# Kernel optimization log

Hardware: AMD Instinct MI355X
Metric: run time of the kernel (lower is better)

Reference implementation:

```python
import jax, jax.numpy as jnp
import numpy as np

N_NODES = 100000
N_EDGES = 1600000
DIM = 128


def setup_inputs() -> dict:
    key = jax.random.key(0)
    k1, k2, k3, k4 = jax.random.split(key, 4)
    x = jax.random.normal(k1, (N_NODES, DIM), dtype=jnp.float32)
    edge_index = jax.random.randint(k2, (2, N_EDGES), 0, N_NODES, dtype=jnp.int64)
    # PyG GCNConv params: Linear weight [out, in] (glorot) and bias [out] (zeros -> use small randn for a non-trivial grad path)
    W = jax.random.normal(k3, (DIM, DIM), dtype=jnp.float32) * (1.0 / np.sqrt(DIM))
    b = jax.random.normal(k4, (DIM,), dtype=jnp.float32) * 0.01
    return {"x": x, "edge_index": edge_index, "W": W, "b": b}


def reference(x, edge_index, W, b):
    # Faithful GCNConv: add self-loops, symmetric deg^-1/2 normalization,
    # linear transform, scatter-add aggregation, bias.
    N = x.shape[0]
    loop = jnp.arange(N, dtype=edge_index.dtype)
    src = jnp.concatenate([edge_index[0], loop])  # [E+N]
    dst = jnp.concatenate([edge_index[1], loop])  # [E+N]

    # degree (with self-loops) on destination nodes
    deg = jax.ops.segment_sum(jnp.ones_like(dst, dtype=x.dtype), dst, num_segments=N)
    dinv = jnp.where(deg > 0, jax.lax.rsqrt(deg), 0.0)
    norm = dinv[src] * dinv[dst]  # [E+N]

    x_lin = x @ W.T  # [N, dim] — PyG applies linear before propagate
    msg = x_lin[src] * norm[:, None]  # [E+N, dim] gather + scale
    out = jax.ops.segment_sum(msg, dst, num_segments=N)  # scatter-add aggregate
    return out + b
```

## Files before the change

kernel.cpp:

```cpp
#include <hip/hip_runtime.h>
#include <hip/hip_bf16.h>


#define DIM 128
#define BINSHIFT 9
#define BINSZ 512
#define NB 196
#define MAXNB 256
#define CAPB 16384
#define WSTRIDE 136
#define SCAT_BLOCKS 256

typedef __attribute__((ext_vector_type(8))) short short8;
typedef __attribute__((ext_vector_type(4))) float f32x4;
typedef __attribute__((ext_vector_type(4))) unsigned short ushort4v;

__device__ inline unsigned short f2bf(float f) {
    unsigned u = __builtin_bit_cast(unsigned, f);
    return (unsigned short)((u + 0x7FFFu + ((u >> 16) & 1u)) >> 16);
}

__device__ inline void bf8_axpy(uint4 v, float s, float* acc) {
    acc[0] = fmaf(s, __builtin_bit_cast(float, v.x << 16), acc[0]);
    acc[1] = fmaf(s, __builtin_bit_cast(float, v.x & 0xFFFF0000u), acc[1]);
    acc[2] = fmaf(s, __builtin_bit_cast(float, v.y << 16), acc[2]);
    acc[3] = fmaf(s, __builtin_bit_cast(float, v.y & 0xFFFF0000u), acc[3]);
    acc[4] = fmaf(s, __builtin_bit_cast(float, v.z << 16), acc[4]);
    acc[5] = fmaf(s, __builtin_bit_cast(float, v.z & 0xFFFF0000u), acc[5]);
    acc[6] = fmaf(s, __builtin_bit_cast(float, v.w << 16), acc[6]);
    acc[7] = fmaf(s, __builtin_bit_cast(float, v.w & 0xFFFF0000u), acc[7]);
}

__global__ __launch_bounds__(256) void scatter_wconv(const int* __restrict__ ei, int E,
                                                     int* __restrict__ binCursor,
                                                     int2* __restrict__ binned,
                                                     const float* __restrict__ W,
                                                     unsigned short* __restrict__ wbf) {
    int t = threadIdx.x;
    if (blockIdx.x >= SCAT_BLOCKS) {
        int base = (blockIdx.x - SCAT_BLOCKS) * 1024 + t * 4;
#pragma unroll
        for (int i = 0; i < 4; ++i) {
            float4 w4 = ((const float4*)W)[base + i];
            ushort4v o; o.x = f2bf(w4.x); o.y = f2bf(w4.y); o.z = f2bf(w4.z); o.w = f2bf(w4.w);
            ((ushort4v*)wbf)[base + i] = o;
        }
        return;
    }
    __shared__ int lh[MAXNB];
    __shared__ int lbase[MAXNB];
    lh[t] = 0;
    __syncthreads();
    int chunk = (E + SCAT_BLOCKS - 1) / SCAT_BLOCKS;
    int base = blockIdx.x * chunk, end = min(E, base + chunk);
    for (int i = base + t; i < end; i += 256)
        atomicAdd(&lh[ei[E + i] >> BINSHIFT], 1);
    __syncthreads();
    if (t < NB) {
        int c = lh[t];
        lbase[t] = c ? atomicAdd(&binCursor[t], c) : 0;
        lh[t] = 0;
    }
    __syncthreads();
    for (int i = base + t; i < end; i += 256) {
        int s = ei[i], d = ei[E + i];
        int b = d >> BINSHIFT;
        int pos = b * CAPB + lbase[b] + atomicAdd(&lh[b], 1);
        binned[pos] = make_int2(s, d);
    }
}


__global__ __launch_bounds__(256) void csr_gemm(const int2* __restrict__ binned,
                                                const int* __restrict__ binCursor,
                                                int* __restrict__ col,
                                                int2* __restrict__ rowinfo,
                                                float* __restrict__ dinv,
                                                const float* __restrict__ x,
                                                const unsigned short* __restrict__ wbf,
                                                unsigned short* __restrict__ xlin, int N) {
    __shared__ unsigned short obuf[4 * 16 * WSTRIDE];
    __shared__ int ldeg[BINSZ], sa[BINSZ], sb[BINSZ], lcur[BINSZ];
    int t = threadIdx.x;

    if (blockIdx.x < NB) {
        int b = blockIdx.x;
        int s0 = b * CAPB;
        int s1 = s0 + binCursor[b];
        for (int i = t; i < BINSZ; i += 256) { ldeg[i] = 0; lcur[i] = 0; }
        __syncthreads();
        for (int i = s0 + t; i < s1; i += 256)
            atomicAdd(&ldeg[binned[i].y & (BINSZ - 1)], 1);
        __syncthreads();
        for (int i = t; i < BINSZ; i += 256) sa[i] = ldeg[i];
        __syncthreads();
        int* src = sa; int* dstp = sb;
        for (int step = 1; step < BINSZ; step <<= 1) {
            for (int i = t; i < BINSZ; i += 256) {
                int v = src[i];
                if (i >= step) v += src[i - step];
                dstp[i] = v;
            }
            __syncthreads();
            int* tmp = src; src = dstp; dstp = tmp;
        }
        for (int i = t; i < BINSZ; i += 256) dstp[i] = src[i] - ldeg[i];
        __syncthreads();
        for (int i = t; i < BINSZ; i += 256) {
            int n = (b << BINSHIFT) + i;
            if (n < N) {
                rowinfo[n] = make_int2(s0 + dstp[i], ldeg[i]);
                dinv[n] = rsqrtf((float)(ldeg[i] + 1));
            }
        }
        for (int i = s0 + t; i < s1; i += 256) {
            int2 e = binned[i];
            int li = e.y & (BINSZ - 1);
            col[s0 + dstp[li] + atomicAdd(&lcur[li], 1)] = e.x;
        }
        return;
    }

    int wid = t >> 6, lane = t & 63;
    int m = lane & 15, quad = lane >> 4;
    int row_base = (blockIdx.x - NB) * 64 + wid * 16;

    f32x4 acc[8];
#pragma unroll
    for (int j = 0; j < 8; ++j) acc[j] = (f32x4){0.f, 0.f, 0.f, 0.f};

    int arow = row_base + m;
    if (arow >= N) arow = N - 1;
    const float* xr = x + (size_t)arow * DIM + quad * 8;

#pragma unroll
    for (int kc = 0; kc < 4; ++kc) {
        float4 a0 = *(const float4*)(xr + kc * 32);
        float4 a1 = *(const float4*)(xr + kc * 32 + 4);
        short8 af;
        af[0] = (short)f2bf(a0.x); af[1] = (short)f2bf(a0.y);
        af[2] = (short)f2bf(a0.z); af[3] = (short)f2bf(a0.w);
        af[4] = (short)f2bf(a1.x); af[5] = (short)f2bf(a1.y);
        af[6] = (short)f2bf(a1.z); af[7] = (short)f2bf(a1.w);
#pragma unroll
        for (int jt = 0; jt < 8; ++jt) {
            short8 bf = *(const short8*)&wbf[(jt * 16 + m) * DIM + kc * 32 + quad * 8];
            acc[jt] = __builtin_amdgcn_mfma_f32_16x16x32_bf16(af, bf, acc[jt], 0, 0, 0);
        }
    }

    unsigned short* ob = &obuf[wid * 16 * WSTRIDE];
#pragma unroll
    for (int jt = 0; jt < 8; ++jt)
#pragma unroll
        for (int r = 0; r < 4; ++r)
            ob[(quad * 4 + r) * WSTRIDE + jt * 16 + m] = f2bf(acc[jt][r]);
#pragma unroll
    for (int it = 0; it < 4; ++it) {
        int idx = it * 64 + lane;
        int r = idx >> 4;
        int cb = idx & 15;
        int grow = row_base + r;
        if (grow < N) {
            short8 v = *(const short8*)&ob[r * WSTRIDE + cb * 8];
            *(short8*)(xlin + (size_t)grow * DIM + cb * 8) = v;
        }
    }
}


__global__ __launch_bounds__(256) void aggregate(const unsigned short* __restrict__ xlin,
                                                 const int* __restrict__ col,
                                                 const int2* __restrict__ rowinfo,
                                                 const float* __restrict__ dinv,
                                                 const float* __restrict__ bias,
                                                 float* __restrict__ out, int N) {
    int node = blockIdx.x * 16 + (threadIdx.x >> 4);
    int lane = threadIdx.x & 15;
    if (node >= N) return;

    float di = dinv[node];
    int2 ri = rowinfo[node];
    int r0 = ri.x, r1 = ri.x + ri.y;

    const uint4* xl = (const uint4*)xlin;
    float acc[8] = {};
    bf8_axpy(xl[(size_t)node * 16 + lane], di, acc);

    for (int i = r0; i < r1; i += 4) {
        int rem = r1 - i;
        int s0 = col[i];
        int s1 = col[rem > 1 ? i + 1 : i];
        int s2 = col[rem > 2 ? i + 2 : i];
        int s3 = col[rem > 3 ? i + 3 : i];
        float d0 = dinv[s0];
        float d1 = rem > 1 ? dinv[s1] : 0.f;
        float d2 = rem > 2 ? dinv[s2] : 0.f;
        float d3 = rem > 3 ? dinv[s3] : 0.f;
        uint4 v0 = xl[(size_t)s0 * 16 + lane];
        uint4 v1 = xl[(size_t)s1 * 16 + lane];
        uint4 v2 = xl[(size_t)s2 * 16 + lane];
        uint4 v3 = xl[(size_t)s3 * 16 + lane];
        bf8_axpy(v0, d0, acc);
        bf8_axpy(v1, d1, acc);
        bf8_axpy(v2, d2, acc);
        bf8_axpy(v3, d3, acc);
    }

    const float4* b4 = (const float4*)(bias + lane * 8);
    float4 bl = b4[0], bh = b4[1];
    float4 olo = make_float4(di * acc[0] + bl.x, di * acc[1] + bl.y,
                             di * acc[2] + bl.z, di * acc[3] + bl.w);
    float4 ohi = make_float4(di * acc[4] + bh.x, di * acc[5] + bh.y,
                             di * acc[6] + bh.z, di * acc[7] + bh.w);
    float4* op = (float4*)(out + (size_t)node * DIM + lane * 8);
    op[0] = olo;
    op[1] = ohi;
}


extern "C" void kernel_launch(void* const* d_in, const int* in_sizes, int n_in,
                              void* d_out, int out_size, void* d_ws, size_t ws_size,
                              hipStream_t stream) {
    const float* x    = (const float*)d_in[0];
    const int*   ei   = (const int*)d_in[1];
    const float* W    = (const float*)d_in[2];
    const float* bias = (const float*)d_in[3];
    float* out = (float*)d_out;

    const int N = in_sizes[0] / DIM;
    const int E = in_sizes[1] / 2;

    char* ws = (char*)d_ws;
    size_t off = 0;
    auto alloc = [&](size_t bytes) { size_t o = off; off = (off + bytes + 255) & ~(size_t)255; return o; };
    unsigned short* xlin = (unsigned short*)(ws + alloc((size_t)N * DIM * 2));
    int2* binned   = (int2*) (ws + alloc((size_t)NB * CAPB * 8));
    int*  col      = (int*)  (ws + alloc((size_t)NB * CAPB * 4));
    int2* rowinfo  = (int2*) (ws + alloc((size_t)N * 8));
    float* dinv    = (float*)(ws + alloc((size_t)N * 4));
    int*  binCursor= (int*)  (ws + alloc(MAXNB * 4));
    unsigned short* wbf = (unsigned short*)(ws + alloc((size_t)DIM * DIM * 2));

    hipMemsetAsync(binCursor, 0, MAXNB * 4, stream);
    scatter_wconv<<<SCAT_BLOCKS + 4, 256, 0, stream>>>(ei, E, binCursor, binned, W, wbf);
    csr_gemm<<<NB + (N + 63) / 64, 256, 0, stream>>>(
        binned, binCursor, col, rowinfo, dinv, x, wbf, xlin, N);
    aggregate<<<(N + 15) / 16, 256, 0, stream>>>(xlin, col, rowinfo, dinv, bias, out, N);
}
```

Baseline: 227.6 us.

## Build CSR via global degree histogram and atomic cursor placement instead of binning

Replaces the two-pass bin-then-sort CSR construction with a global per-node degree histogram (global atomics), a per-bin scan kernel that writes row starts and dinv, and an atomic-cursor placement of source indices fused into the GEMM launch. This drops the intermediate binned edge array and its extra read/write pass. In exchange it relies on heavily contended global atomics over 1.6M edges, adds a kernel launch and an N-sized memset, and makes the order of neighbours within each row nondeterministic.

Result: slower. 334.6 us (+47.0%).

```diff
diff --git a/kernel.cpp b/kernel.cpp
--- a/kernel.cpp
+++ b/kernel.cpp
@@ -6,10 +6,8 @@
 #define BINSHIFT 9
 #define BINSZ 512
 #define NB 196
-#define MAXNB 256
 #define CAPB 16384
 #define WSTRIDE 136
-#define SCAT_BLOCKS 256
 
 typedef __attribute__((ext_vector_type(8))) short short8;
 typedef __attribute__((ext_vector_type(4))) float f32x4;
@@ -31,14 +29,15 @@
     acc[7] = fmaf(s, __builtin_bit_cast(float, v.w & 0xFFFF0000u), acc[7]);
 }
 
-__global__ __launch_bounds__(256) void scatter_wconv(const int* __restrict__ ei, int E,
-                                                     int* __restrict__ binCursor,
-                                                     int2* __restrict__ binned,
-                                                     const float* __restrict__ W,
-                                                     unsigned short* __restrict__ wbf) {
+__global__ __launch_bounds__(256) void hist_wconv(const int* __restrict__ ei, int E,
+                                                  int* __restrict__ deg,
+                                                  const float* __restrict__ W,
+                                                  unsigned short* __restrict__ wbf) {
     int t = threadIdx.x;
-    if (blockIdx.x >= SCAT_BLOCKS) {
-        int base = (blockIdx.x - SCAT_BLOCKS) * 1024 + t * 4;
+    int E4 = E >> 2;
+    int nh = (E4 + 255) >> 8;
+    if ((int)blockIdx.x >= nh) {
+        int base = ((int)blockIdx.x - nh) * 1024 + t * 4;
 #pragma unroll
         for (int i = 0; i < 4; ++i) {
             float4 w4 = ((const float4*)W)[base + i];
@@ -47,83 +46,85 @@
         }
         return;
     }
-    __shared__ int lh[MAXNB];
-    __shared__ int lbase[MAXNB];
-    lh[t] = 0;
+    int i4 = blockIdx.x * 256 + t;
+    if (i4 < E4) {
+        int4 d = ((const int4*)(ei + E))[i4];
+        atomicAdd(&deg[d.x], 1);
+        atomicAdd(&deg[d.y], 1);
+        atomicAdd(&deg[d.z], 1);
+        atomicAdd(&deg[d.w], 1);
+    }
+    if (blockIdx.x == 0 && t < (E & 3))
+        atomicAdd(&deg[ei[E + (E4 << 2) + t]], 1);
+}
+
+__global__ __launch_bounds__(256) void csrscan(int* __restrict__ degc,
+                                               int2* __restrict__ rowinfo,
+                                               float* __restrict__ dinv, int N) {
+    __shared__ int ldeg[BINSZ], sa[BINSZ], sb[BINSZ];
+    int t = threadIdx.x;
+    int b = blockIdx.x;
+    for (int i = t; i < BINSZ; i += 256) {
+        int n = (b << BINSHIFT) + i;
+        ldeg[i] = (n < N) ? degc[n] : 0;
+    }
     __syncthreads();
-    int chunk = (E + SCAT_BLOCKS - 1) / SCAT_BLOCKS;
-    int base = blockIdx.x * chunk, end = min(E, base + chunk);
-    for (int i = base + t; i < end; i += 256)
-        atomicAdd(&lh[ei[E + i] >> BINSHIFT], 1);
+    for (int i = t; i < BINSZ; i += 256) sa[i] = ldeg[i];
     __syncthreads();
-    if (t < NB) {
-        int c = lh[t];
-        lbase[t] = c ? atomicAdd(&binCursor[t], c) : 0;
-        lh[t] = 0;
-    }
-    __syncthreads();
-    for (int i = base + t; i < end; i += 256) {
-        int s = ei[i], d = ei[E + i];
-        int b = d >> BINSHIFT;
-        int pos = b * CAPB + lbase[b] + atomicAdd(&lh[b], 1);
-        binned[pos] = make_int2(s, d);
-    }
-}
-
-
-__global__ __launch_bounds__(256) void csr_gemm(const int2* __restrict__ binned,
-                                                const int* __restrict__ binCursor,
-                                                int* __restrict__ col,
-                                                int2* __restrict__ rowinfo,
-                                                float* __restrict__ dinv,
-                                                const float* __restrict__ x,
-                                                const unsigned short* __restrict__ wbf,
-                                                unsigned short* __restrict__ xlin, int N) {
+    int* src = sa; int* dstp = sb;
+    for (int step = 1; step < BINSZ; step <<= 1) {
+        for (int i = t; i < BINSZ; i += 256) {
+            int v = src[i];
+            if (i >= step) v += src[i - step];
+            dstp[i] = v;
+        }
+        __syncthreads();
+        int* tmp = src; src = dstp; dstp = tmp;
+    }
+    for (int i = t; i < BINSZ; i += 256) {
+        int n = (b << BINSHIFT) + i;
+        if (n < N) {
+            int d = ldeg[i];
+            int start = b * CAPB + src[i] - d;
+            rowinfo[n] = make_int2(start, d);
+            dinv[n] = rsqrtf((float)(d + 1));
+            degc[n] = start;
+        }
+    }
+}
+
+__global__ __launch_bounds__(256) void gemm_place(const float* __restrict__ x,
+                                                  const unsigned short* __restrict__ wbf,
+                                                  unsigned short* __restrict__ xlin,
+                                                  const int* __restrict__ ei, int E,
+                                                  int* __restrict__ cursor,
+                                                  int* __restrict__ col, int N) {
     __shared__ unsigned short obuf[4 * 16 * WSTRIDE];
-    __shared__ int ldeg[BINSZ], sa[BINSZ], sb[BINSZ], lcur[BINSZ];
     int t = threadIdx.x;
-
-    if (blockIdx.x < NB) {
-        int b = blockIdx.x;
-        int s0 = b * CAPB;
-        int s1 = s0 + binCursor[b];
-        for (int i = t; i < BINSZ; i += 256) { ldeg[i] = 0; lcur[i] = 0; }
-        __syncthreads();
-        for (int i = s0 + t; i < s1; i += 256)
-            atomicAdd(&ldeg[binned[i].y & (BINSZ - 1)], 1);
-        __syncthreads();
-        for (int i = t; i < BINSZ; i += 256) sa[i] = ldeg[i];
-        __syncthreads();
-        int* src = sa; int* dstp = sb;
-        for (int step = 1; step < BINSZ; step <<= 1) {
-            for (int i = t; i < BINSZ; i += 256) {
-                int v = src[i];
-                if (i >= step) v += src[i - step];
-                dstp[i] = v;
-            }
-            __syncthreads();
-            int* tmp = src; src = dstp; dstp = tmp;
-        }
-        for (int i = t; i < BINSZ; i += 256) dstp[i] = src[i] - ldeg[i];
-        __syncthreads();
-        for (int i = t; i < BINSZ; i += 256) {
-            int n = (b << BINSHIFT) + i;
-            if (n < N) {
-                rowinfo[n] = make_int2(s0 + dstp[i], ldeg[i]);
-                dinv[n] = rsqrtf((float)(ldeg[i] + 1));
-            }
-        }
-        for (int i = s0 + t; i < s1; i += 256) {
-            int2 e = binned[i];
-            int li = e.y & (BINSZ - 1);
-            col[s0 + dstp[li] + atomicAdd(&lcur[li], 1)] = e.x;
+    int GB = (N + 63) >> 6;
+
+    if ((int)blockIdx.x >= GB) {
+        int pb = (int)blockIdx.x - GB;
+        int E4 = E >> 2;
+        int i4 = pb * 256 + t;
+        if (i4 < E4) {
+            int4 s = ((const int4*)ei)[i4];
+            int4 d = ((const int4*)(ei + E))[i4];
+            col[atomicAdd(&cursor[d.x], 1)] = s.x;
+            col[atomicAdd(&cursor[d.y], 1)] = s.y;
+            col[atomicAdd(&cursor[d.z], 1)] = s.z;
+            col[atomicAdd(&cursor[d.w], 1)] = s.w;
+        }
+        if (pb == 0 && t < (E & 3)) {
+            int i = (E4 << 2) + t;
+            col[atomicAdd(&cursor[ei[E + i]], 1)] = ei[i];
         }
         return;
     }
 
     int wid = t >> 6, lane = t & 63;
     int m = lane & 15, quad = lane >> 4;
-    int row_base = (blockIdx.x - NB) * 64 + wid * 16;
+    int row_base = blockIdx.x * 64 + wid * 16;
 
     f32x4 acc[8];
 #pragma unroll
@@ -235,16 +236,19 @@
     size_t off = 0;
     auto alloc = [&](size_t bytes) { size_t o = off; off = (off + bytes + 255) & ~(size_t)255; return o; };
     unsigned short* xlin = (unsigned short*)(ws + alloc((size_t)N * DIM * 2));
-    int2* binned   = (int2*) (ws + alloc((size_t)NB * CAPB * 8));
     int*  col      = (int*)  (ws + alloc((size_t)NB * CAPB * 4));
     int2* rowinfo  = (int2*) (ws + alloc((size_t)N * 8));
     float* dinv    = (float*)(ws + alloc((size_t)N * 4));
-    int*  binCursor= (int*)  (ws + alloc(MAXNB * 4));
+    int*  degc     = (int*)  (ws + alloc((size_t)N * 4));
     unsigned short* wbf = (unsigned short*)(ws + alloc((size_t)DIM * DIM * 2));
 
-    hipMemsetAsync(binCursor, 0, MAXNB * 4, stream);
-    scatter_wconv<<<SCAT_BLOCKS + 4, 256, 0, stream>>>(ei, E, binCursor, binned, W, wbf);
-    csr_gemm<<<NB + (N + 63) / 64, 256, 0, stream>>>(
-        binned, binCursor, col, rowinfo, dinv, x, wbf, xlin, N);
+    int E4 = E >> 2;
+    int HB = (E4 + 255) >> 8;
+    int GB = (N + 63) >> 6;
+
+    hipMemsetAsync(degc, 0, (size_t)N * 4, stream);
+    hist_wconv<<<HB + 4, 256, 0, stream>>>(ei, E, degc, W, wbf);
+    csrscan<<<NB, 256, 0, stream>>>(degc, rowinfo, dinv, N);
+    gemm_place<<<GB + HB, 256, 0, stream>>>(x, wbf, xlin, ei, E, degc, col, N);
     aggregate<<<(N + 15) / 16, 256, 0, stream>>>(xlin, col, rowinfo, dinv, bias, out, N);
 }
```

## Regroup kernels: fuse edge scatter with GEMM, split CSR build into own kernel

Applied to the files above, without the earlier changes.

Moves the dense x·W GEMM into the same launch as the edge binning scatter, and moves the per-bin CSR construction into a separate 512-thread kernel that runs afterwards. The W bf16 conversion becomes its own tiny launch. The aim is to overlap the bandwidth-bound GEMM with the atomic-heavy scatter and to stop CSR blocks from sharing a launch with GEMM blocks. It also widens the CSR scan to one thread per node, and it adds a kernel launch plus a block barrier before the xlin store.

New measurement: 229.5 us. No clear change (+0.8%).

```diff
diff --git a/kernel.cpp b/kernel.cpp
--- a/kernel.cpp
+++ b/kernel.cpp
@@ -31,99 +31,55 @@
     acc[7] = fmaf(s, __builtin_bit_cast(float, v.w & 0xFFFF0000u), acc[7]);
 }
 
-__global__ __launch_bounds__(256) void scatter_wconv(const int* __restrict__ ei, int E,
-                                                     int* __restrict__ binCursor,
-                                                     int2* __restrict__ binned,
-                                                     const float* __restrict__ W,
-                                                     unsigned short* __restrict__ wbf) {
+__global__ __launch_bounds__(256) void wconv(const float* __restrict__ W,
+                                             unsigned short* __restrict__ wbf) {
+    int base = blockIdx.x * 1024 + threadIdx.x * 4;
+#pragma unroll
+    for (int i = 0; i < 4; ++i) {
+        float4 w4 = ((const float4*)W)[base + i];
+        ushort4v o; o.x = f2bf(w4.x); o.y = f2bf(w4.y); o.z = f2bf(w4.z); o.w = f2bf(w4.w);
+        ((ushort4v*)wbf)[base + i] = o;
+    }
+}
+
+__global__ __launch_bounds__(256) void scatter_gemm(const int* __restrict__ ei, int E,
+                                                    int* __restrict__ binCursor,
+                                                    int2* __restrict__ binned,
+                                                    const float* __restrict__ x,
+                                                    const unsigned short* __restrict__ wbf,
+                                                    unsigned short* __restrict__ xlin, int N) {
+    __shared__ __align__(16) char smem[4 * 16 * WSTRIDE * 2];
     int t = threadIdx.x;
-    if (blockIdx.x >= SCAT_BLOCKS) {
-        int base = (blockIdx.x - SCAT_BLOCKS) * 1024 + t * 4;
-#pragma unroll
-        for (int i = 0; i < 4; ++i) {
-            float4 w4 = ((const float4*)W)[base + i];
-            ushort4v o; o.x = f2bf(w4.x); o.y = f2bf(w4.y); o.z = f2bf(w4.z); o.w = f2bf(w4.w);
-            ((ushort4v*)wbf)[base + i] = o;
+
+    if (blockIdx.x < SCAT_BLOCKS) {
+        int* lh = (int*)smem;
+        int* lbase = lh + MAXNB;
+        lh[t] = 0;
+        __syncthreads();
+        int chunk = (E + SCAT_BLOCKS - 1) / SCAT_BLOCKS;
+        int base = blockIdx.x * chunk, end = min(E, base + chunk);
+        for (int i = base + t; i < end; i += 256)
+            atomicAdd(&lh[ei[E + i] >> BINSHIFT], 1);
+        __syncthreads();
+        if (t < NB) {
+            int c = lh[t];
+            lbase[t] = c ? atomicAdd(&binCursor[t], c) : 0;
+            lh[t] = 0;
+        }
+        __syncthreads();
+        for (int i = base + t; i < end; i += 256) {
+            int s = ei[i], d = ei[E + i];
+            int b = d >> BINSHIFT;
+            int pos = b * CAPB + lbase[b] + atomicAdd(&lh[b], 1);
+            binned[pos] = make_int2(s, d);
         }
         return;
     }
-    __shared__ int lh[MAXNB];
-    __shared__ int lbase[MAXNB];
-    lh[t] = 0;
-    __syncthreads();
-    int chunk = (E + SCAT_BLOCKS - 1) / SCAT_BLOCKS;
-    int base = blockIdx.x * chunk, end = min(E, base + chunk);
-    for (int i = base + t; i < end; i += 256)
-        atomicAdd(&lh[ei[E + i] >> BINSHIFT], 1);
-    __syncthreads();
-    if (t < NB) {
-        int c = lh[t];
-        lbase[t] = c ? atomicAdd(&binCursor[t], c) : 0;
-        lh[t] = 0;
-    }
-    __syncthreads();
-    for (int i = base + t; i < end; i += 256) {
-        int s = ei[i], d = ei[E + i];
-        int b = d >> BINSHIFT;
-        int pos = b * CAPB + lbase[b] + atomicAdd(&lh[b], 1);
-        binned[pos] = make_int2(s, d);
-    }
-}
-
-
-__global__ __launch_bounds__(256) void csr_gemm(const int2* __restrict__ binned,
-                                                const int* __restrict__ binCursor,
-                                                int* __restrict__ col,
-                                                int2* __restrict__ rowinfo,
-                                                float* __restrict__ dinv,
-                                                const float* __restrict__ x,
-                                                const unsigned short* __restrict__ wbf,
-                                                unsigned short* __restrict__ xlin, int N) {
-    __shared__ unsigned short obuf[4 * 16 * WSTRIDE];
-    __shared__ int ldeg[BINSZ], sa[BINSZ], sb[BINSZ], lcur[BINSZ];
-    int t = threadIdx.x;
-
-    if (blockIdx.x < NB) {
-        int b = blockIdx.x;
-        int s0 = b * CAPB;
-        int s1 = s0 + binCursor[b];
-        for (int i = t; i < BINSZ; i += 256) { ldeg[i] = 0; lcur[i] = 0; }
-        __syncthreads();
-        for (int i = s0 + t; i < s1; i += 256)
-            atomicAdd(&ldeg[binned[i].y & (BINSZ - 1)], 1);
-        __syncthreads();
-        for (int i = t; i < BINSZ; i += 256) sa[i] = ldeg[i];
-        __syncthreads();
-        int* src = sa; int* dstp = sb;
-        for (int step = 1; step < BINSZ; step <<= 1) {
-            for (int i = t; i < BINSZ; i += 256) {
-                int v = src[i];
-                if (i >= step) v += src[i - step];
-                dstp[i] = v;
-            }
-            __syncthreads();
-            int* tmp = src; src = dstp; dstp = tmp;
-        }
-        for (int i = t; i < BINSZ; i += 256) dstp[i] = src[i] - ldeg[i];
-        __syncthreads();
-        for (int i = t; i < BINSZ; i += 256) {
-            int n = (b << BINSHIFT) + i;
-            if (n < N) {
-                rowinfo[n] = make_int2(s0 + dstp[i], ldeg[i]);
-                dinv[n] = rsqrtf((float)(ldeg[i] + 1));
-            }
-        }
-        for (int i = s0 + t; i < s1; i += 256) {
-            int2 e = binned[i];
-            int li = e.y & (BINSZ - 1);
-            col[s0 + dstp[li] + atomicAdd(&lcur[li], 1)] = e.x;
-        }
-        return;
-    }
-
+
+    unsigned short* obuf = (unsigned short*)smem;
     int wid = t >> 6, lane = t & 63;
     int m = lane & 15, quad = lane >> 4;
-    int row_base = (blockIdx.x - NB) * 64 + wid * 16;
+    int row_base = (blockIdx.x - SCAT_BLOCKS) * 64 + wid * 16;
 
     f32x4 acc[8];
 #pragma unroll
@@ -155,6 +111,7 @@
 #pragma unroll
         for (int r = 0; r < 4; ++r)
             ob[(quad * 4 + r) * WSTRIDE + jt * 16 + m] = f2bf(acc[jt][r]);
+    __syncthreads();
 #pragma unroll
     for (int it = 0; it < 4; ++it) {
         int idx = it * 64 + lane;
@@ -165,6 +122,48 @@
             short8 v = *(const short8*)&ob[r * WSTRIDE + cb * 8];
             *(short8*)(xlin + (size_t)grow * DIM + cb * 8) = v;
         }
+    }
+}
+
+__global__ __launch_bounds__(512) void csr_build(const int2* __restrict__ binned,
+                                                 const int* __restrict__ binCursor,
+                                                 int* __restrict__ col,
+                                                 int2* __restrict__ rowinfo,
+                                                 float* __restrict__ dinv, int N) {
+    __shared__ int ldeg[BINSZ], sa[BINSZ], sb[BINSZ], lcur[BINSZ];
+    int t = threadIdx.x;
+    int b = blockIdx.x;
+    int s0 = b * CAPB;
+    int s1 = s0 + binCursor[b];
+
+    ldeg[t] = 0; lcur[t] = 0;
+    __syncthreads();
+    for (int i = s0 + t; i < s1; i += 512)
+        atomicAdd(&ldeg[binned[i].y & (BINSZ - 1)], 1);
+    __syncthreads();
+    sa[t] = ldeg[t];
+    __syncthreads();
+    int* src = sa; int* dstp = sb;
+    for (int step = 1; step < BINSZ; step <<= 1) {
+        int v = src[t];
+        if (t >= step) v += src[t - step];
+        dstp[t] = v;
+        __syncthreads();
+        int* tmp = src; src = dstp; dstp = tmp;
+    }
+    int d = ldeg[t];
+    int startoff = src[t] - d;
+    int n = (b << BINSHIFT) + t;
+    if (n < N) {
+        rowinfo[n] = make_int2(s0 + startoff, d);
+        dinv[n] = rsqrtf((float)(d + 1));
+    }
+    dstp[t] = startoff;
+    __syncthreads();
+    for (int i = s0 + t; i < s1; i += 512) {
+        int2 e = binned[i];
+        int li = e.y & (BINSZ - 1);
+        col[s0 + dstp[li] + atomicAdd(&lcur[li], 1)] = e.x;
     }
 }
 
@@ -242,9 +241,11 @@
     int*  binCursor= (int*)  (ws + alloc(MAXNB * 4));
     unsigned short* wbf = (unsigned short*)(ws + alloc((size_t)DIM * DIM * 2));
 
+    int GB = (N + 63) / 64;
+
     hipMemsetAsync(binCursor, 0, MAXNB * 4, stream);
-    scatter_wconv<<<SCAT_BLOCKS + 4, 256, 0, stream>>>(ei, E, binCursor, binned, W, wbf);
-    csr_gemm<<<NB + (N + 63) / 64, 256, 0, stream>>>(
-        binned, binCursor, col, rowinfo, dinv, x, wbf, xlin, N);
+    wconv<<<4, 256, 0, stream>>>(W, wbf);
+    scatter_gemm<<<SCAT_BLOCKS + GB, 256, 0, stream>>>(ei, E, binCursor, binned, x, wbf, xlin, N);
+    csr_build<<<NB, 512, 0, stream>>>(binned, binCursor, col, rowinfo, dinv, N);
     aggregate<<<(N + 15) / 16, 256, 0, stream>>>(xlin, col, rowinfo, dinv, bias, out, N);
 }
```
